# Optimization experiments

Hardware: AMD Instinct MI355X
Metric: run time of the kernel (lower is better)

Reference implementation:

```python
import jax, jax.numpy as jnp
import numpy as np

L, K, B, CS, NS = 100000, 128, 16384, 8, 20
N_EPOCHS = 10
SIG = 1.0
LOG_SQRT_2PI = 0.9189385332046727  # 0.5*log(2*pi)


def normal_logprob(x, sig):
    # Normal(0, sig).log_prob(x), elementwise
    return -0.5 * (x / sig) ** 2 - jnp.log(sig) - LOG_SQRT_2PI


def setup_inputs() -> dict:
    key = jax.random.key(0)
    k1, k2, k3, k4, k5 = jax.random.split(key, 5)
    contexts = jax.random.randint(k1, (B, CS), 0, L + 1)   # context_embed has L+1 rows (padding row L)
    targets = jax.random.randint(k2, (B, 1), 0, L)
    neg_idx = jax.random.randint(k3, (B, NS), 0, L)        # stands in for torch.multinomial draws
    target_W = jax.random.normal(k4, (L, K), dtype=jnp.float32) / K
    context_W = jax.random.normal(k5, (L + 1, K), dtype=jnp.float32) / K
    return {"contexts": contexts, "targets": targets, "neg_idx": neg_idx,
            "target_W": target_W, "context_W": context_W}


def reference(contexts, targets, neg_idx, target_W, context_W):
    # gathers
    pos_context = context_W[contexts]                       # [B, CS, K]
    ctx_sum = pos_context.sum(axis=1)                       # [B, K]
    pos_target = target_W[targets[:, 0]]                    # [B, K]
    # positive logits, Bernoulli log_prob at value=1: -softplus(-eta)
    pos_eta = jnp.einsum('bk,bk->b', pos_target, ctx_sum)[:, None]   # [B, 1]
    ll_pos = (-jax.nn.softplus(-pos_eta)).sum(axis=0)       # [1]
    # negative logits, Bernoulli log_prob at value=0: -softplus(eta)
    neg_target = target_W[neg_idx]                          # [B, NS, K]
    neg_eta = jnp.einsum('bnk,bk->bn', neg_target, ctx_sum) # [B, NS]
    ll_neg = (-jax.nn.softplus(neg_eta)).sum()              # scalar
    # Gaussian prior over the full tables (computed on .data in torch -> no grad)
    log_prior = (normal_logprob(jax.lax.stop_gradient(context_W), SIG).sum()
                 + normal_logprob(jax.lax.stop_gradient(target_W), SIG).sum())
    log_likelihood = ll_pos + ll_neg                        # [1]
    loss = -(N_EPOCHS * log_likelihood + log_prior)         # [1]
    return loss
```

## Files before the change

### kernel.cpp

```cpp
#include <hip/hip_runtime.h>

#define L_SZ 100000
#define K_DIM 128
#define B_SZ 16384
#define CS_SZ 8
#define NS_SZ 20
#define NEPOCH 10
#define LOG_SQRT_2PI 0.9189385332046727

typedef float f32x4 __attribute__((ext_vector_type(4)));

__device__ __forceinline__ float softplus_f(float x) {
    return fmaxf(x, 0.0f) + __logf(1.0f + __expf(-fabsf(x)));
}

__global__ __launch_bounds__(256) void fused_kernel(
    const int* __restrict__ contexts, const int* __restrict__ targets,
    const int* __restrict__ neg_idx, const float* __restrict__ tW,
    const float* __restrict__ cW,
    double* __restrict__ pll, double* __restrict__ pprior)
{
    const int lane = threadIdx.x & 63;
    const int wave = threadIdx.x >> 6;
    const int j = lane & 15;
    const int g = lane >> 4;

    const int n_mine = 4 * j + g;
    const bool valid = (n_mine < 21);
    const float sgn = (n_mine == 0) ? -1.0f : 1.0f;

    const int b = __builtin_amdgcn_readfirstlane(blockIdx.x * 4 + wave);

    float4 r0[6], r1[6];
    #pragma unroll
    for (int s = 0; s < 6; ++s) {
        const int n = 4 * s + g;
        int t;
        if (n == 0)       t = targets[b];
        else if (n < 21)  t = neg_idx[b * NS_SZ + (n - 1)];
        else              t = neg_idx[b * NS_SZ];
        const float4* r = reinterpret_cast<const float4*>(
            &tW[(size_t)t * K_DIM + j * 8]);
        r0[s] = r[0]; r1[s] = r[1];
    }

    float4 s0 = {0.f, 0.f, 0.f, 0.f}, s1 = {0.f, 0.f, 0.f, 0.f};
    #pragma unroll
    for (int c = 0; c < CS_SZ; ++c) {
        const int idx = contexts[b * CS_SZ + c];
        const float4* r = reinterpret_cast<const float4*>(
            &cW[(size_t)idx * K_DIM + j * 8]);
        const float4 a = r[0], d = r[1];
        s0.x += a.x; s0.y += a.y; s0.z += a.z; s0.w += a.w;
        s1.x += d.x; s1.y += d.y; s1.z += d.z; s1.w += d.w;
    }

    float lacc = 0.0f;
    float keep = 0.0f;
    #pragma unroll
    for (int s = 0; s < 6; ++s) {
        const float4 a = r0[s], d = r1[s];
        float p = a.x * s0.x + a.y * s0.y + a.z * s0.z + a.w * s0.w
                + d.x * s1.x + d.y * s1.y + d.z * s1.z + d.w * s1.w;
        p += __shfl_xor(p, 1, 16);
        p += __shfl_xor(p, 2, 16);
        p += __shfl_xor(p, 4, 16);
        p += __shfl_xor(p, 8, 16);
        keep = (j == s) ? p : keep;
    }
    lacc = valid ? softplus_f(sgn * keep) : 0.0f;

    const int NT4 = (L_SZ * K_DIM) / 4;
    const int NC4 = ((L_SZ + 1) * K_DIM) / 4;
    const int tid = blockIdx.x * blockDim.x + threadIdx.x;
    const int stride = gridDim.x * blockDim.x;

    float pacc = 0.0f;
    const f32x4* t4 = reinterpret_cast<const f32x4*>(tW);
    for (int i = tid; i < NT4; i += stride) {
        const f32x4 v = __builtin_nontemporal_load(&t4[i]);
        pacc += v.x * v.x + v.y * v.y + v.z * v.z + v.w * v.w;
    }
    const f32x4* c4 = reinterpret_cast<const f32x4*>(cW);
    for (int i = tid; i < NC4; i += stride) {
        const f32x4 v = __builtin_nontemporal_load(&c4[i]);
        pacc += v.x * v.x + v.y * v.y + v.z * v.z + v.w * v.w;
    }

    #pragma unroll
    for (int o = 32; o; o >>= 1) {
        lacc += __shfl_xor(lacc, o, 64);
        pacc += __shfl_xor(pacc, o, 64);
    }
    __shared__ float sl[4], sp[4];
    if (lane == 0) { sl[wave] = lacc; sp[wave] = pacc; }
    __syncthreads();
    if (threadIdx.x == 0) {
        pll[blockIdx.x]    = (double)(sl[0] + sl[1] + sl[2] + sl[3]);
        pprior[blockIdx.x] = (double)(sp[0] + sp[1] + sp[2] + sp[3]);
    }
}

__global__ __launch_bounds__(256) void finalize_kernel(
    const double* __restrict__ pll, int nll,
    const double* __restrict__ pprior, int nprior,
    float* __restrict__ out)
{
    double a = 0.0, p = 0.0;
    for (int i = threadIdx.x; i < nll; i += 256) a += pll[i];
    for (int i = threadIdx.x; i < nprior; i += 256) p += pprior[i];

    __shared__ double sA[256], sP[256];
    sA[threadIdx.x] = a; sP[threadIdx.x] = p;
    __syncthreads();
    for (int s = 128; s > 0; s >>= 1) {
        if (threadIdx.x < s) {
            sA[threadIdx.x] += sA[threadIdx.x + s];
            sP[threadIdx.x] += sP[threadIdx.x + s];
        }
        __syncthreads();
    }
    if (threadIdx.x == 0) {
        const double C = (double)((2LL * L_SZ + 1) * K_DIM) * LOG_SQRT_2PI;
        const double loss = (double)NEPOCH * sA[0] + 0.5 * sP[0] + C;
        out[0] = (float)loss;
    }
}

extern "C" void kernel_launch(void* const* d_in, const int* in_sizes, int n_in,
                              void* d_out, int out_size, void* d_ws, size_t ws_size,
                              hipStream_t stream) {
    const int*   contexts = (const int*)d_in[0];
    const int*   targets  = (const int*)d_in[1];
    const int*   neg_idx  = (const int*)d_in[2];
    const float* tW       = (const float*)d_in[3];
    const float* cW       = (const float*)d_in[4];
    float* out = (float*)d_out;

    double* pll    = (double*)d_ws;
    double* pprior = pll + 4096;

    fused_kernel<<<4096, 256, 0, stream>>>(contexts, targets, neg_idx,
                                           tW, cW, pll, pprior);
    finalize_kernel<<<1, 256, 0, stream>>>(pll, 4096, pprior, 4096, out);
}
```

Measured before the change: 63.92 us.

## Stream tables before gathers so gathers hit cache, fuse finalize via last-block atomic

Moves the full-table prior sweep ahead of the embedding gathers and drops the nontemporal hints, so gathered rows are more likely to be served from cache instead of DRAM. Index loads are hoisted before the sweep, and the gather layout changes to two float4 chunks offset by 64. The separate finalize kernel is replaced by a last-block-done pattern using an atomic counter, which needs a memset before launch. This trades one kernel launch for a memset plus atomic and threadfence overhead, and cache reuse depends on the tables (about 100 MB) fitting in the cache.

Result: slower. 192.8 us (+201.6%).

```diff
diff --git a/kernel.cpp b/kernel.cpp
--- a/kernel.cpp
+++ b/kernel.cpp
@@ -7,6 +7,7 @@
 #define NS_SZ 20
 #define NEPOCH 10
 #define LOG_SQRT_2PI 0.9189385332046727
+#define NBLOCKS 4096
 
 typedef float f32x4 __attribute__((ext_vector_type(4)));
 
@@ -18,7 +19,8 @@
     const int* __restrict__ contexts, const int* __restrict__ targets,
     const int* __restrict__ neg_idx, const float* __restrict__ tW,
     const float* __restrict__ cW,
-    double* __restrict__ pll, double* __restrict__ pprior)
+    double* __restrict__ pll, double* __restrict__ pprior,
+    unsigned int* __restrict__ counter, float* __restrict__ out)
 {
     const int lane = threadIdx.x & 63;
     const int wave = threadIdx.x >> 6;
@@ -31,7 +33,11 @@
 
     const int b = __builtin_amdgcn_readfirstlane(blockIdx.x * 4 + wave);
 
-    float4 r0[6], r1[6];
+    int ctxi[CS_SZ];
+    #pragma unroll
+    for (int c = 0; c < CS_SZ; ++c) ctxi[c] = contexts[b * CS_SZ + c];
+
+    int tidx[6];
     #pragma unroll
     for (int s = 0; s < 6; ++s) {
         const int n = 4 * s + g;
@@ -39,23 +45,44 @@
         if (n == 0)       t = targets[b];
         else if (n < 21)  t = neg_idx[b * NS_SZ + (n - 1)];
         else              t = neg_idx[b * NS_SZ];
-        const float4* r = reinterpret_cast<const float4*>(
-            &tW[(size_t)t * K_DIM + j * 8]);
-        r0[s] = r[0]; r1[s] = r[1];
+        tidx[s] = t;
+    }
+
+    const int NT4 = (L_SZ * K_DIM) / 4;
+    const int NC4 = ((L_SZ + 1) * K_DIM) / 4;
+    const int tid = blockIdx.x * blockDim.x + threadIdx.x;
+    const int stride = gridDim.x * blockDim.x;
+
+    float pacc = 0.0f;
+    const f32x4* t4 = reinterpret_cast<const f32x4*>(tW);
+    for (int i = tid; i < NT4; i += stride) {
+        const f32x4 v = t4[i];
+        pacc += v.x * v.x + v.y * v.y + v.z * v.z + v.w * v.w;
+    }
+    const f32x4* c4 = reinterpret_cast<const f32x4*>(cW);
+    for (int i = tid; i < NC4; i += stride) {
+        const f32x4 v = c4[i];
+        pacc += v.x * v.x + v.y * v.y + v.z * v.z + v.w * v.w;
+    }
+
+    float4 r0[6], r1[6];
+    #pragma unroll
+    for (int s = 0; s < 6; ++s) {
+        const float* base = &tW[(size_t)tidx[s] * K_DIM];
+        r0[s] = *reinterpret_cast<const float4*>(base + 4 * j);
+        r1[s] = *reinterpret_cast<const float4*>(base + 64 + 4 * j);
     }
 
     float4 s0 = {0.f, 0.f, 0.f, 0.f}, s1 = {0.f, 0.f, 0.f, 0.f};
     #pragma unroll
     for (int c = 0; c < CS_SZ; ++c) {
-        const int idx = contexts[b * CS_SZ + c];
-        const float4* r = reinterpret_cast<const float4*>(
-            &cW[(size_t)idx * K_DIM + j * 8]);
-        const float4 a = r[0], d = r[1];
+        const float* base = &cW[(size_t)ctxi[c] * K_DIM];
+        const float4 a = *reinterpret_cast<const float4*>(base + 4 * j);
+        const float4 d = *reinterpret_cast<const float4*>(base + 64 + 4 * j);
         s0.x += a.x; s0.y += a.y; s0.z += a.z; s0.w += a.w;
         s1.x += d.x; s1.y += d.y; s1.z += d.z; s1.w += d.w;
     }
 
-    float lacc = 0.0f;
     float keep = 0.0f;
     #pragma unroll
     for (int s = 0; s < 6; ++s) {
@@ -68,24 +95,7 @@
         p += __shfl_xor(p, 8, 16);
         keep = (j == s) ? p : keep;
     }
-    lacc = valid ? softplus_f(sgn * keep) : 0.0f;
-
-    const int NT4 = (L_SZ * K_DIM) / 4;
-    const int NC4 = ((L_SZ + 1) * K_DIM) / 4;
-    const int tid = blockIdx.x * blockDim.x + threadIdx.x;
-    const int stride = gridDim.x * blockDim.x;
-
-    float pacc = 0.0f;
-    const f32x4* t4 = reinterpret_cast<const f32x4*>(tW);
-    for (int i = tid; i < NT4; i += stride) {
-        const f32x4 v = __builtin_nontemporal_load(&t4[i]);
-        pacc += v.x * v.x + v.y * v.y + v.z * v.z + v.w * v.w;
-    }
-    const f32x4* c4 = reinterpret_cast<const f32x4*>(cW);
-    for (int i = tid; i < NC4; i += stride) {
-        const f32x4 v = __builtin_nontemporal_load(&c4[i]);
-        pacc += v.x * v.x + v.y * v.y + v.z * v.z + v.w * v.w;
-    }
+    float lacc = valid ? softplus_f(sgn * keep) : 0.0f;
 
     #pragma unroll
     for (int o = 32; o; o >>= 1) {
@@ -95,35 +105,38 @@
     __shared__ float sl[4], sp[4];
     if (lane == 0) { sl[wave] = lacc; sp[wave] = pacc; }
     __syncthreads();
+
+    __shared__ bool amLast;
     if (threadIdx.x == 0) {
         pll[blockIdx.x]    = (double)(sl[0] + sl[1] + sl[2] + sl[3]);
         pprior[blockIdx.x] = (double)(sp[0] + sp[1] + sp[2] + sp[3]);
+        __threadfence();
+        const unsigned t = atomicAdd(counter, 1u);
+        amLast = (t == (unsigned)(gridDim.x - 1));
     }
-}
+    __syncthreads();
 
-__global__ __launch_bounds__(256) void finalize_kernel(
-    const double* __restrict__ pll, int nll,
-    const double* __restrict__ pprior, int nprior,
-    float* __restrict__ out)
-{
-    double a = 0.0, p = 0.0;
-    for (int i = threadIdx.x; i < nll; i += 256) a += pll[i];
-    for (int i = threadIdx.x; i < nprior; i += 256) p += pprior[i];
-
-    __shared__ double sA[256], sP[256];
-    sA[threadIdx.x] = a; sP[threadIdx.x] = p;
-    __syncthreads();
-    for (int s = 128; s > 0; s >>= 1) {
-        if (threadIdx.x < s) {
-            sA[threadIdx.x] += sA[threadIdx.x + s];
-            sP[threadIdx.x] += sP[threadIdx.x + s];
+    if (amLast) {
+        __threadfence();
+        double a = 0.0, p = 0.0;
+        for (int i = threadIdx.x; i < NBLOCKS; i += 256) {
+            a += pll[i];
+            p += pprior[i];
         }
+        __shared__ double sA[256], sP[256];
+        sA[threadIdx.x] = a; sP[threadIdx.x] = p;
         __syncthreads();
-    }
-    if (threadIdx.x == 0) {
-        const double C = (double)((2LL * L_SZ + 1) * K_DIM) * LOG_SQRT_2PI;
-        const double loss = (double)NEPOCH * sA[0] + 0.5 * sP[0] + C;
-        out[0] = (float)loss;
+        for (int s = 128; s > 0; s >>= 1) {
+            if (threadIdx.x < s) {
+                sA[threadIdx.x] += sA[threadIdx.x + s];
+                sP[threadIdx.x] += sP[threadIdx.x + s];
+            }
+            __syncthreads();
+        }
+        if (threadIdx.x == 0) {
+            const double C = (double)((2LL * L_SZ + 1) * K_DIM) * LOG_SQRT_2PI;
+            out[0] = (float)((double)NEPOCH * sA[0] + 0.5 * sP[0] + C);
+        }
     }
 }
 
@@ -137,10 +150,12 @@
     const float* cW       = (const float*)d_in[4];
     float* out = (float*)d_out;
 
-    double* pll    = (double*)d_ws;
-    double* pprior = pll + 4096;
+    double* pll        = (double*)d_ws;
+    double* pprior     = pll + NBLOCKS;
+    unsigned* counter  = (unsigned*)(pprior + NBLOCKS);
 
-    fused_kernel<<<4096, 256, 0, stream>>>(contexts, targets, neg_idx,
-                                           tW, cW, pll, pprior);
-    finalize_kernel<<<1, 256, 0, stream>>>(pll, 4096, pprior, 4096, out);
+    hipMemsetAsync(counter, 0, sizeof(unsigned), stream);
+
+    fused_kernel<<<NBLOCKS, 256, 0, stream>>>(contexts, targets, neg_idx,
+                                              tW, cW, pll, pprior, counter, out);
 }
```
